# Optimization experiments

Measured on AMD Instinct MI355X. Metric: run time of the kernel, lower is better.

## Reference

```python
import jax, jax.numpy as jnp
import numpy as np


def _bilinear_grid_sample(fea, grid):
    """torch.nn.functional.grid_sample, mode=bilinear, padding_mode=zeros, align_corners=False.
    fea: (B,C,H,W); grid: (B,Hg,Wg,2) with xy in [-1,1]. Returns (B,C,Hg,Wg)."""
    B, C, H, W = fea.shape
    Hg, Wg = grid.shape[1], grid.shape[2]
    gx, gy = grid[..., 0], grid[..., 1]
    # unnormalize (align_corners=False)
    x = ((gx + 1.0) * W - 1.0) * 0.5
    y = ((gy + 1.0) * H - 1.0) * 0.5
    x0 = jnp.floor(x); y0 = jnp.floor(y)
    x1 = x0 + 1.0;     y1 = y0 + 1.0
    wx1 = x - x0; wx0 = 1.0 - wx1
    wy1 = y - y0; wy0 = 1.0 - wy1
    flat = fea.reshape(B, C, H * W)

    def corner(xi, yi, w):
        valid = (xi >= 0) & (xi <= W - 1) & (yi >= 0) & (yi <= H - 1)
        xi_c = jnp.clip(xi, 0, W - 1).astype(jnp.int32)
        yi_c = jnp.clip(yi, 0, H - 1).astype(jnp.int32)
        idx = (yi_c * W + xi_c).reshape(B, 1, Hg * Wg)
        v = jnp.take_along_axis(flat, jnp.broadcast_to(idx, (B, C, Hg * Wg)), axis=2)
        return v * (w * valid.astype(fea.dtype)).reshape(B, 1, Hg * Wg)

    out = (corner(x0, y0, wx0 * wy0) + corner(x1, y0, wx1 * wy0)
           + corner(x0, y1, wx0 * wy1) + corner(x1, y1, wx1 * wy1))
    return out.reshape(B, C, Hg, Wg)


def _conv1d_k1(x, W, b):
    # x: (B,Cin,N), W: (Cout,Cin), b: (Cout,) -> (B,Cout,N)
    return jnp.einsum('oc,bcn->bon', W, x) + b[None, :, None]


def setup_inputs() -> dict:
    key = jax.random.key(0)
    ks = jax.random.split(key, 8)
    B, C, H, W = 4, 16, 90, 160
    N_s, N_anchor, N_y = 8, 200, 20
    scale = 8
    fea = jax.random.normal(ks[0], (B, C, H, W), dtype=jnp.float32)
    sampled_3d_points = jax.random.normal(ks[1], (N_s, B, N_anchor, N_y, 4), dtype=jnp.float32)
    # 2D pixel coords at full resolution: x in [0, W*scale), y in [0, H*scale)
    u = jax.random.uniform(ks[2], (N_s, B, N_anchor, N_y, 2), dtype=jnp.float32)
    points_2d_coord = u * jnp.array([W * scale, H * scale], dtype=jnp.float32)
    W_local = jax.random.normal(ks[3], (16, 16), dtype=jnp.float32) * 0.25
    b_local = jax.random.normal(ks[4], (16,), dtype=jnp.float32) * 0.01
    W_emb = jax.random.normal(ks[5], (256, 4), dtype=jnp.float32) * 0.5
    b_emb = jax.random.normal(ks[6], (256,), dtype=jnp.float32) * 0.01
    return {"fea": fea, "sampled_3d_points": sampled_3d_points,
            "points_2d_coord": points_2d_coord,
            "W_local": W_local, "b_local": b_local,
            "W_emb": W_emb, "b_emb": b_emb, "scale": scale}


def reference(fea, sampled_3d_points, points_2d_coord, W_local, b_local, W_emb, b_emb, scale):
    B, C, H, W = fea.shape
    N_s, _, N_anchor, N_y, _ = points_2d_coord.shape
    # normalize 2D coords to [-1,1] grid
    norm_weight = jnp.array([1.0 / W, 1.0 / H], dtype=fea.dtype)
    ner = (points_2d_coord / scale) * norm_weight * 2.0 - 1.0
    ner = jnp.transpose(ner, (1, 0, 2, 3, 4)).reshape(B, N_s * N_anchor, N_y, 2)
    local_fea = _bilinear_grid_sample(fea, ner)            # (B,C,N_s*N_anchor,N_y)
    local_fea = local_fea.reshape(B, C, -1)                # (B,C,N)
    local_fea = _conv1d_k1(local_fea, W_local, b_local)    # (B,16,N)
    # point embedding: permute(1,4,0,2,3) -> (B,4,N_s,N_anchor,N_y)
    sp = jnp.transpose(sampled_3d_points, (1, 4, 0, 2, 3)).reshape(B, 4, -1)
    embedded_points = _conv1d_k1(sp, W_emb, b_emb)         # (B,256,N)
    return (embedded_points, local_fea)
```

## Files before the change

kernel.cpp:

```cpp
#include <hip/hip_runtime.h>

#define B_    4
#define C_    16
#define H_    90
#define W_    160
#define NS_   8
#define NA_   200
#define NY_   20
#define NPB_  (NS_*NA_*NY_)
#define NPB4_ (NPB_/4)
#define CO_   256
#define EMB_ELEMS ((size_t)B_*CO_*NPB_)
#define SCALE_F 8.0f
#define HW_   (H_*W_)

#define TILES_    (NPB_/256)
#define LOC_BLOCKS (B_*TILES_)
#define OCHUNKS_  4
#define EMB_BLOCKS (B_*TILES_*OCHUNKS_)
#define TOTAL_BLOCKS (LOC_BLOCKS + EMB_BLOCKS)

#define SMEM_FLOATS 4368

__global__ __launch_bounds__(256) void fused_local_emb_kernel(
    const float*  __restrict__ fea,
    const float4* __restrict__ sp3d,
    const float2* __restrict__ pc2d,
    const float*  __restrict__ W_local,
    const float*  __restrict__ b_local,
    const float4* __restrict__ W_emb,
    const float*  __restrict__ b_emb,
    float* __restrict__ out)
{
    __shared__ float smem[SMEM_FLOATS];
    const int tid = threadIdx.x;
    const int idx = blockIdx.x;
    const int l  = tid & 63;
    const int wv = tid >> 6;

    if (idx >= LOC_BLOCKS) {
        const int eid  = idx - LOC_BLOCKS;
        const int b    = eid / (TILES_*OCHUNKS_);
        const int rem0 = eid - b*(TILES_*OCHUNKS_);
        const int tile = rem0 / OCHUNKS_;
        const int oc   = rem0 - tile*OCHUNKS_;

        float* sPx = smem;
        float* sPy = smem + 256;
        float* sPz = smem + 512;
        float* sPw = smem + 768;
        float4* sWe4 = (float4*)(smem + 1024);
        float*  sbe  = smem + 1280;

        if (tid < 64) {
            sWe4[tid] = W_emb[oc*64 + tid];
            sbe[tid]  = b_emb[oc*64 + tid];
        }

        const int n   = tile*256 + tid;
        const int s   = n / (NA_*NY_);
        const int rem = n - s*(NA_*NY_);
        const int a   = rem / NY_;
        const int yy  = rem - a*NY_;
        const float4 p = sp3d[((s*B_ + b)*NA_ + a)*NY_ + yy];
        sPx[tid] = p.x; sPy[tid] = p.y; sPz[tid] = p.z; sPw[tid] = p.w;
        __syncthreads();

        const float4 PX = ((const float4*)sPx)[l];
        const float4 PY = ((const float4*)sPy)[l];
        const float4 PZ = ((const float4*)sPz)[l];
        const float4 PW = ((const float4*)sPw)[l];

        float4* eo4 = (float4*)(out + (size_t)b*CO_*NPB_);
        const int obase = wv*16;
        const int ostart = oc*64 + obase;
#pragma unroll
        for (int k = 0; k < 16; ++k) {
            const float4 w = sWe4[obase + k];
            const float bb = sbe[obase + k];
            float4 r;
            r.x = fmaf(w.w,PW.x, fmaf(w.z,PZ.x, fmaf(w.y,PY.x, fmaf(w.x,PX.x, bb))));
            r.y = fmaf(w.w,PW.y, fmaf(w.z,PZ.y, fmaf(w.y,PY.y, fmaf(w.x,PX.y, bb))));
            r.z = fmaf(w.w,PW.z, fmaf(w.z,PZ.z, fmaf(w.y,PY.z, fmaf(w.x,PX.z, bb))));
            r.w = fmaf(w.w,PW.w, fmaf(w.z,PZ.w, fmaf(w.y,PY.w, fmaf(w.x,PX.w, bb))));
            eo4[(size_t)(ostart + k)*NPB4_ + tile*64 + l] = r;
        }
        return;
    }

    float* sWl = smem;
    float* sbl = smem + 256;
    float* sV  = smem + 272;

    sWl[tid] = W_local[tid];
    if (tid < 16) sbl[tid] = b_local[tid];

    const int b    = idx / TILES_;
    const int tile = idx - b*TILES_;
    const int n    = tile*256 + tid;

    const int s   = n / (NA_*NY_);
    const int rem = n - s*(NA_*NY_);
    const int a   = rem / NY_;
    const int yy  = rem - a*NY_;

    const float2 pc = pc2d[((s*B_ + b)*NA_ + a)*NY_ + yy];

    const float gx = (pc.x / SCALE_F) * (1.0f/(float)W_) * 2.0f - 1.0f;
    const float gy = (pc.y / SCALE_F) * (1.0f/(float)H_) * 2.0f - 1.0f;
    const float xf = ((gx + 1.0f) * (float)W_ - 1.0f) * 0.5f;
    const float yf = ((gy + 1.0f) * (float)H_ - 1.0f) * 0.5f;

    const float x0f = floorf(xf), y0f = floorf(yf);
    const float x1f = x0f + 1.0f, y1f = y0f + 1.0f;
    const float wx1 = xf - x0f, wx0 = 1.0f - wx1;
    const float wy1 = yf - y0f, wy0 = 1.0f - wy1;

    const float vx0 = (x0f >= 0.0f && x0f <= (float)(W_-1)) ? 1.0f : 0.0f;
    const float vx1 = (x1f >= 0.0f && x1f <= (float)(W_-1)) ? 1.0f : 0.0f;
    const float vy0 = (y0f >= 0.0f && y0f <= (float)(H_-1)) ? 1.0f : 0.0f;
    const float vy1 = (y1f >= 0.0f && y1f <= (float)(H_-1)) ? 1.0f : 0.0f;

    const int xi0 = (int)fminf(fmaxf(x0f, 0.0f), (float)(W_-1));
    const int xi1 = (int)fminf(fmaxf(x1f, 0.0f), (float)(W_-1));
    const int yi0 = (int)fminf(fmaxf(y0f, 0.0f), (float)(H_-1));
    const int yi1 = (int)fminf(fmaxf(y1f, 0.0f), (float)(H_-1));

    const float w00 = wx0*wy0*vx0*vy0;
    const float w01 = wx1*wy0*vx1*vy0;
    const float w10 = wx0*wy1*vx0*vy1;
    const float w11 = wx1*wy1*vx1*vy1;

    const int i00 = yi0*W_ + xi0;
    const int i01 = yi0*W_ + xi1;
    const int i10 = yi1*W_ + xi0;
    const int i11 = yi1*W_ + xi1;

    const float* fb = fea + b*(C_*HW_);
    float f00[16], f01[16], f10[16], f11[16];
#pragma unroll
    for (int c = 0; c < 16; ++c) {
        const float* fc = fb + c*HW_;
        f00[c] = fc[i00];
        f01[c] = fc[i01];
        f10[c] = fc[i10];
        f11[c] = fc[i11];
    }

    float v[16];
#pragma unroll
    for (int c = 0; c < 16; ++c)
        v[c] = w00*f00[c] + w01*f01[c] + w10*f10[c] + w11*f11[c];
#pragma unroll
    for (int c = 0; c < 16; ++c)
        sV[c*256 + tid] = v[c];

    __syncthreads();

    float4 acc[4];
#pragma unroll
    for (int k = 0; k < 4; ++k) {
        const float bk = sbl[4*wv + k];
        acc[k].x = bk; acc[k].y = bk; acc[k].z = bk; acc[k].w = bk;
    }
#pragma unroll
    for (int c = 0; c < 16; ++c) {
        const float4 sv = ((const float4*)(sV + c*256))[l];
#pragma unroll
        for (int k = 0; k < 4; ++k) {
            const float wl = sWl[(4*wv + k)*16 + c];
            acc[k].x = fmaf(wl, sv.x, acc[k].x);
            acc[k].y = fmaf(wl, sv.y, acc[k].y);
            acc[k].z = fmaf(wl, sv.z, acc[k].z);
            acc[k].w = fmaf(wl, sv.w, acc[k].w);
        }
    }
    float4* lo4 = (float4*)(out + EMB_ELEMS + (size_t)b*16*NPB_ + tile*256);
#pragma unroll
    for (int k = 0; k < 4; ++k)
        lo4[(4*wv + k)*NPB4_ + l] = acc[k];
}

extern "C" void kernel_launch(void* const* d_in, const int* in_sizes, int n_in,
                              void* d_out, int out_size, void* d_ws, size_t ws_size,
                              hipStream_t stream) {
    const float* fea     = (const float*)d_in[0];
    const float4* sp3d   = (const float4*)d_in[1];
    const float2* pc2d   = (const float2*)d_in[2];
    const float* W_local = (const float*)d_in[3];
    const float* b_local = (const float*)d_in[4];
    const float4* W_emb  = (const float4*)d_in[5];
    const float* b_emb   = (const float*)d_in[6];

    dim3 grid(TOTAL_BLOCKS);
    dim3 block(256);
    fused_local_emb_kernel<<<grid, block, 0, stream>>>(
        fea, sp3d, pc2d, W_local, b_local, W_emb, b_emb, (float*)d_out);
}
```

Baseline: 42.81 us.

## Retile embedding blocks into 1280-point chunks with 16-output groups

Embedding blocks now cover 1280 points and 16 output channels each, instead of 256 points and 64 channels. Each wave writes 4 output rows, each as a contiguous 5KB span, so the store pattern becomes longer runs per row. The cost is that every block reloads the 3D points for its chunk, and reuse of those points across output channels goes down. The grid shape and the amount of shared-memory reads per output also change.

```diff
diff --git a/kernel.cpp b/kernel.cpp
--- a/kernel.cpp
+++ b/kernel.cpp
@@ -14,13 +14,19 @@
 #define SCALE_F 8.0f
 #define HW_   (H_*W_)
 
-#define TILES_    (NPB_/256)
+#define TILES_     (NPB_/256)
 #define LOC_BLOCKS (B_*TILES_)
-#define OCHUNKS_  4
-#define EMB_BLOCKS (B_*TILES_*OCHUNKS_)
+
+#define CHUNK_PTS  1280
+#define NCHUNKS    (NPB_/CHUNK_PTS)
+#define OG_SIZE    16
+#define NOG        (CO_/OG_SIZE)
+#define EMB_BLOCKS (B_*NCHUNKS*NOG)
 #define TOTAL_BLOCKS (LOC_BLOCKS + EMB_BLOCKS)
-
-#define SMEM_FLOATS 4368
+#define CHUNK_G    (CHUNK_PTS/4)
+#define GSTEPS     (CHUNK_G/64)
+
+#define SMEM_FLOATS 5200
 
 __global__ __launch_bounds__(256) void fused_local_emb_kernel(
     const float*  __restrict__ fea,
@@ -39,51 +45,59 @@
     const int wv = tid >> 6;
 
     if (idx >= LOC_BLOCKS) {
-        const int eid  = idx - LOC_BLOCKS;
-        const int b    = eid / (TILES_*OCHUNKS_);
-        const int rem0 = eid - b*(TILES_*OCHUNKS_);
-        const int tile = rem0 / OCHUNKS_;
-        const int oc   = rem0 - tile*OCHUNKS_;
+        const int eid   = idx - LOC_BLOCKS;
+        const int b     = eid / (NCHUNKS*NOG);
+        const int rem0  = eid - b*(NCHUNKS*NOG);
+        const int chunk = rem0 / NOG;
+        const int og    = rem0 - chunk*NOG;
 
         float* sPx = smem;
-        float* sPy = smem + 256;
-        float* sPz = smem + 512;
-        float* sPw = smem + 768;
-        float4* sWe4 = (float4*)(smem + 1024);
-        float*  sbe  = smem + 1280;
-
-        if (tid < 64) {
-            sWe4[tid] = W_emb[oc*64 + tid];
-            sbe[tid]  = b_emb[oc*64 + tid];
-        }
-
-        const int n   = tile*256 + tid;
-        const int s   = n / (NA_*NY_);
-        const int rem = n - s*(NA_*NY_);
-        const int a   = rem / NY_;
-        const int yy  = rem - a*NY_;
-        const float4 p = sp3d[((s*B_ + b)*NA_ + a)*NY_ + yy];
-        sPx[tid] = p.x; sPy[tid] = p.y; sPz[tid] = p.z; sPw[tid] = p.w;
+        float* sPy = smem + CHUNK_PTS;
+        float* sPz = smem + 2*CHUNK_PTS;
+        float* sPw = smem + 3*CHUNK_PTS;
+        float4* sWe4 = (float4*)(smem + 4*CHUNK_PTS);
+        float*  sbe  = smem + 4*CHUNK_PTS + 64;
+
+        if (tid < OG_SIZE) {
+            sWe4[tid] = W_emb[og*OG_SIZE + tid];
+            sbe[tid]  = b_emb[og*OG_SIZE + tid];
+        }
+
+#pragma unroll
+        for (int j = 0; j < 5; ++j) {
+            const int pn = chunk*CHUNK_PTS + j*256 + tid;
+            const int s  = pn / (NA_*NY_);
+            const int r  = pn - s*(NA_*NY_);
+            const float4 p = sp3d[s*(B_*NA_*NY_) + b*(NA_*NY_) + r];
+            sPx[j*256 + tid] = p.x;
+            sPy[j*256 + tid] = p.y;
+            sPz[j*256 + tid] = p.z;
+            sPw[j*256 + tid] = p.w;
+        }
         __syncthreads();
 
-        const float4 PX = ((const float4*)sPx)[l];
-        const float4 PY = ((const float4*)sPy)[l];
-        const float4 PZ = ((const float4*)sPz)[l];
-        const float4 PW = ((const float4*)sPw)[l];
-
-        float4* eo4 = (float4*)(out + (size_t)b*CO_*NPB_);
-        const int obase = wv*16;
-        const int ostart = oc*64 + obase;
-#pragma unroll
-        for (int k = 0; k < 16; ++k) {
-            const float4 w = sWe4[obase + k];
-            const float bb = sbe[obase + k];
-            float4 r;
-            r.x = fmaf(w.w,PW.x, fmaf(w.z,PZ.x, fmaf(w.y,PY.x, fmaf(w.x,PX.x, bb))));
-            r.y = fmaf(w.w,PW.y, fmaf(w.z,PZ.y, fmaf(w.y,PY.y, fmaf(w.x,PX.y, bb))));
-            r.z = fmaf(w.w,PW.z, fmaf(w.z,PZ.z, fmaf(w.y,PY.z, fmaf(w.x,PX.z, bb))));
-            r.w = fmaf(w.w,PW.w, fmaf(w.z,PZ.w, fmaf(w.y,PY.w, fmaf(w.x,PX.w, bb))));
-            eo4[(size_t)(ostart + k)*NPB4_ + tile*64 + l] = r;
+        float4* eb4 = (float4*)(out + (size_t)b*CO_*NPB_);
+#pragma unroll
+        for (int k = 0; k < 4; ++k) {
+            const int m = wv*4 + k;
+            const int o = og*OG_SIZE + m;
+            const float4 w  = sWe4[m];
+            const float  bb = sbe[m];
+            float4* row4 = eb4 + (size_t)o*NPB4_ + chunk*CHUNK_G;
+#pragma unroll
+            for (int g = 0; g < GSTEPS; ++g) {
+                const int gi = g*64 + l;
+                const float4 PX = ((const float4*)sPx)[gi];
+                const float4 PY = ((const float4*)sPy)[gi];
+                const float4 PZ = ((const float4*)sPz)[gi];
+                const float4 PW = ((const float4*)sPw)[gi];
+                float4 r;
+                r.x = fmaf(w.w,PW.x, fmaf(w.z,PZ.x, fmaf(w.y,PY.x, fmaf(w.x,PX.x, bb))));
+                r.y = fmaf(w.w,PW.y, fmaf(w.z,PZ.y, fmaf(w.y,PY.y, fmaf(w.x,PX.y, bb))));
+                r.z = fmaf(w.w,PW.z, fmaf(w.z,PZ.z, fmaf(w.y,PY.z, fmaf(w.x,PX.z, bb))));
+                r.w = fmaf(w.w,PW.w, fmaf(w.z,PZ.w, fmaf(w.y,PY.w, fmaf(w.x,PX.w, bb))));
+                row4[gi] = r;
+            }
         }
         return;
     }
```

Measured after the change: 43.63 us. Within noise of the previous version (+1.9%).
